# Performance work log

Measured on AMD Instinct MI355X. Metric: run time of the kernel, lower is better.

Reference implementation:

```python
import jax, jax.numpy as jnp
import numpy as np

BLOCK = 64          # block_size
R = 64              # number of OFT blocks (r)
N_ELEM = BLOCK * (BLOCK - 1) // 2  # 2016 upper-triangular elements per block
TOKENS = 8192       # batch*seq tokens
IN_FEATURES = R * BLOCK  # 4096
NUM_TERMS = 5       # num_cayley_neumann_terms

_ROWS, _COLS = jnp.triu_indices(BLOCK, k=1)


def _skew_symmetric(vec):
    # vec: [r, n_elements] -> [r, BLOCK, BLOCK] skew-symmetric
    m = jnp.zeros((vec.shape[0], BLOCK, BLOCK), dtype=vec.dtype)
    m = m.at[:, _ROWS, _COLS].set(vec)
    return m - jnp.swapaxes(m, -2, -1)


def _cayley_neumann(weight):
    # Neumann approximation of Cayley transform:
    # R = I + 2*Q + 2*Q^2 + ... + 2*Q^(NUM_TERMS-1)
    Q = _skew_symmetric(weight)                      # [r, B, B]
    eye = jnp.eye(BLOCK, dtype=weight.dtype)
    rot = eye[None, :, :] + 2.0 * Q
    Q_pow = Q
    for _ in range(2, NUM_TERMS):
        Q_pow = jnp.einsum('rij,rjk->rik', Q_pow, Q)
        rot = rot + 2.0 * Q_pow
    return rot                                        # [r, B, B]


def setup_inputs() -> dict:
    key = jax.random.key(0)
    k1, k2 = jax.random.split(key)
    x = jax.random.normal(k1, (TOKENS, IN_FEATURES), dtype=jnp.float32)
    # OFT weights start near zero (rotation ~ identity); small scale keeps
    # the Neumann series well-conditioned.
    weight = jax.random.normal(k2, (R, N_ELEM), dtype=jnp.float32) * 0.02
    return {"x": x, "weight": weight}


def reference(x, weight):
    rot = _cayley_neumann(weight)                      # [r, B, B]
    xr = x.reshape(x.shape[0], R, BLOCK)               # [n, r, B]
    out = jnp.einsum('nrk,rkc->nrc', xr, rot)          # block-diag rotation
    return out.reshape(x.shape)
```

## Files before the change

### kernel.cpp

```cpp
#include <hip/hip_runtime.h>


#define NELEM 2016

__device__ __forceinline__ int triu_off(int i) {
    return i * 63 - (i * (i - 1)) / 2;
}

__device__ __forceinline__ float skew_val(const float* __restrict__ wr, int i, int j) {
    if (i < j) return  wr[triu_off(i) + (j - i - 1)];
    if (i > j) return -wr[triu_off(j) + (i - j - 1)];
    return 0.f;
}

__global__ __launch_bounds__(256) void oft_rot_kernel(const float* __restrict__ w,
                                                      float* __restrict__ rot) {
    __shared__ float Q[64][64];
    __shared__ float Pl[2][16][65];

    const int r    = blockIdx.x;
    const int tile = blockIdx.y;
    const float* __restrict__ wr = w + r * NELEM;
    const int tid = threadIdx.x;
    const int il  = tid >> 4;
    const int j0  = (tid & 15) << 2;
    const int gi  = tile * 16 + il;

#pragma unroll
    for (int m = 0; m < 4; ++m) {
        const int i = il + 16 * m;
#pragma unroll
        for (int t = 0; t < 4; ++t)
            Q[i][j0 + t] = skew_val(wr, i, j0 + t);
    }
    __syncthreads();

    float racc[4];
#pragma unroll
    for (int t = 0; t < 4; ++t) {
        const float qv = Q[gi][j0 + t];
        Pl[0][il][j0 + t] = qv;
        racc[t] = (gi == j0 + t ? 1.f : 0.f) + 2.f * qv;
    }
    __syncthreads();

    int cur = 0;
#pragma unroll
    for (int p = 2; p < 5; ++p) {
        float a0 = 0.f, a1 = 0.f, a2 = 0.f, a3 = 0.f;
#pragma unroll 8
        for (int k = 0; k < 64; ++k) {
            const float  pv = Pl[cur][il][k];
            const float4 qv = *(const float4*)&Q[k][j0];
            a0 = fmaf(pv, qv.x, a0);
            a1 = fmaf(pv, qv.y, a1);
            a2 = fmaf(pv, qv.z, a2);
            a3 = fmaf(pv, qv.w, a3);
        }
        Pl[cur ^ 1][il][j0 + 0] = a0;
        Pl[cur ^ 1][il][j0 + 1] = a1;
        Pl[cur ^ 1][il][j0 + 2] = a2;
        Pl[cur ^ 1][il][j0 + 3] = a3;
        racc[0] += 2.f * a0;
        racc[1] += 2.f * a1;
        racc[2] += 2.f * a2;
        racc[3] += 2.f * a3;
        __syncthreads();
        cur ^= 1;
    }

    *(float4*)&rot[(size_t)r * 4096 + gi * 64 + j0] =
        make_float4(racc[0], racc[1], racc[2], racc[3]);
}

__global__ __launch_bounds__(256, 3) void oft_apply_kernel(const float* __restrict__ x,
                                                           const float* __restrict__ rot,
                                                           float* __restrict__ out) {
    __shared__ float rotS[64][64];
    __shared__ float xs[128][65];

    const int r   = blockIdx.x;
    const int tok0 = blockIdx.y * 128;
    const int tid = threadIdx.x;

    {
        const float4* __restrict__ src = (const float4*)(rot + (size_t)r * 4096);
        float4* dst = (float4*)&rotS[0][0];
#pragma unroll
        for (int p = 0; p < 4; ++p)
            dst[p * 256 + tid] = src[p * 256 + tid];
    }
#pragma unroll
    for (int p = 0; p < 8; ++p) {
        const int f   = p * 256 + tid;
        const int row = f >> 4;
        const int c   = (f & 15) << 2;
        const float4 v = *(const float4*)(x + (size_t)(tok0 + row) * 4096 + r * 64 + c);
        xs[row][c + 0] = v.x;
        xs[row][c + 1] = v.y;
        xs[row][c + 2] = v.z;
        xs[row][c + 3] = v.w;
    }
    __syncthreads();

    const int cq = tid & 15;
    const int tq = tid >> 4;
    const int c0 = cq << 2;
    const float* __restrict__ xbase = &xs[tq * 8][0];

    float acc[8][4];
#pragma unroll
    for (int m = 0; m < 8; ++m)
#pragma unroll
        for (int t = 0; t < 4; ++t) acc[m][t] = 0.f;

#pragma unroll 8
    for (int k = 0; k < 64; ++k) {
        const float4 rv = *(const float4*)&rotS[k][c0];
#pragma unroll
        for (int m = 0; m < 8; ++m) {
            const float xv = xbase[m * 65 + k];
            acc[m][0] = fmaf(xv, rv.x, acc[m][0]);
            acc[m][1] = fmaf(xv, rv.y, acc[m][1]);
            acc[m][2] = fmaf(xv, rv.z, acc[m][2]);
            acc[m][3] = fmaf(xv, rv.w, acc[m][3]);
        }
    }

#pragma unroll
    for (int m = 0; m < 8; ++m) {
        const int n = tok0 + tq * 8 + m;
        *(float4*)(out + (size_t)n * 4096 + r * 64 + c0) =
            make_float4(acc[m][0], acc[m][1], acc[m][2], acc[m][3]);
    }
}

extern "C" void kernel_launch(void* const* d_in, const int* in_sizes, int n_in,
                              void* d_out, int out_size, void* d_ws, size_t ws_size,
                              hipStream_t stream) {
    const float* x = (const float*)d_in[0];
    const float* w = (const float*)d_in[1];
    float* out = (float*)d_out;
    float* rot = (float*)d_ws;

    oft_rot_kernel<<<dim3(64, 4), 256, 0, stream>>>(w, rot);
    oft_apply_kernel<<<dim3(64, 64), 256, 0, stream>>>(x, rot, out);
}
```

Before: 250.0 us.

## Use split-bf16 MFMA for block-diagonal rotation apply with prepacked fragments

The rotation kernel now writes each rotation matrix as high and low bf16 halves, prepacked in MFMA B-fragment layout. The apply kernel drops the shared-memory fp32 FMA loop. Each wave loads x straight into registers, splits it into bf16 hi/lo, and runs three bf16 MFMA products per k-slab (hi*hi + hi*lo + lo*hi) to keep close to fp32 accuracy on matrix cores. This trades extra MFMA work and scattered scalar output stores for removing the LDS staging and scalar FMA throughput limits.

Result: no change. 253.6 us (+1.4%).

```diff
diff --git a/kernel.cpp b/kernel.cpp
--- a/kernel.cpp
+++ b/kernel.cpp
@@ -2,6 +2,9 @@
 
 
 #define NELEM 2016
+
+typedef __attribute__((ext_vector_type(8))) short bfrag8;
+typedef __attribute__((ext_vector_type(4))) float f32x4;
 
 __device__ __forceinline__ int triu_off(int i) {
     return i * 63 - (i * (i - 1)) / 2;
@@ -13,8 +16,17 @@
     return 0.f;
 }
 
+__device__ __forceinline__ void bsplit(float v, short& h, short& l) {
+    const unsigned u = __float_as_uint(v);
+    h = (short)(u >> 16);
+    const float resid = v - __uint_as_float(u & 0xffff0000u);
+    const unsigned ur = __float_as_uint(resid);
+    l = (short)((ur + 0x7fffu + ((ur >> 16) & 1u)) >> 16);
+}
+
 __global__ __launch_bounds__(256) void oft_rot_kernel(const float* __restrict__ w,
-                                                      float* __restrict__ rot) {
+                                                      unsigned short* __restrict__ bh,
+                                                      unsigned short* __restrict__ bl) {
     __shared__ float Q[64][64];
     __shared__ float Pl[2][16][65];
 
@@ -69,69 +81,83 @@
         cur ^= 1;
     }
 
-    *(float4*)&rot[(size_t)r * 4096 + gi * 64 + j0] =
-        make_float4(racc[0], racc[1], racc[2], racc[3]);
+    const int s    = gi >> 5;
+    const int jj   = gi & 7;
+    const int lhi  = ((gi >> 3) & 3) << 4;
+#pragma unroll
+    for (int t = 0; t < 4; ++t) {
+        const int j    = j0 + t;
+        const int ct   = j >> 4;
+        const int lane = lhi + (j & 15);
+        const int off  = (((r * 4 + ct) * 2 + s) * 64 + lane) * 8 + jj;
+        short h, l;
+        bsplit(racc[t], h, l);
+        bh[off] = (unsigned short)h;
+        bl[off] = (unsigned short)l;
+    }
 }
 
-__global__ __launch_bounds__(256, 3) void oft_apply_kernel(const float* __restrict__ x,
-                                                           const float* __restrict__ rot,
-                                                           float* __restrict__ out) {
-    __shared__ float rotS[64][64];
-    __shared__ float xs[128][65];
+__global__ __launch_bounds__(256) void oft_apply_kernel(const float* __restrict__ x,
+                                                        const unsigned short* __restrict__ bh,
+                                                        const unsigned short* __restrict__ bl,
+                                                        float* __restrict__ out) {
+    const int tid  = threadIdx.x;
+    const int w    = tid >> 6;
+    const int l    = tid & 63;
+    const int lrow = l & 15;
+    const int lk   = l >> 4;
+    const int r     = blockIdx.x;
+    const int chunk = blockIdx.y;
 
-    const int r   = blockIdx.x;
-    const int tok0 = blockIdx.y * 128;
-    const int tid = threadIdx.x;
-
-    {
-        const float4* __restrict__ src = (const float4*)(rot + (size_t)r * 4096);
-        float4* dst = (float4*)&rotS[0][0];
+    bfrag8 Bh[4][2], Bl[4][2];
 #pragma unroll
-        for (int p = 0; p < 4; ++p)
-            dst[p * 256 + tid] = src[p * 256 + tid];
-    }
+    for (int ct = 0; ct < 4; ++ct)
 #pragma unroll
-    for (int p = 0; p < 8; ++p) {
-        const int f   = p * 256 + tid;
-        const int row = f >> 4;
-        const int c   = (f & 15) << 2;
-        const float4 v = *(const float4*)(x + (size_t)(tok0 + row) * 4096 + r * 64 + c);
-        xs[row][c + 0] = v.x;
-        xs[row][c + 1] = v.y;
-        xs[row][c + 2] = v.z;
-        xs[row][c + 3] = v.w;
-    }
-    __syncthreads();
-
-    const int cq = tid & 15;
-    const int tq = tid >> 4;
-    const int c0 = cq << 2;
-    const float* __restrict__ xbase = &xs[tq * 8][0];
-
-    float acc[8][4];
-#pragma unroll
-    for (int m = 0; m < 8; ++m)
-#pragma unroll
-        for (int t = 0; t < 4; ++t) acc[m][t] = 0.f;
-
-#pragma unroll 8
-    for (int k = 0; k < 64; ++k) {
-        const float4 rv = *(const float4*)&rotS[k][c0];
-#pragma unroll
-        for (int m = 0; m < 8; ++m) {
-            const float xv = xbase[m * 65 + k];
-            acc[m][0] = fmaf(xv, rv.x, acc[m][0]);
-            acc[m][1] = fmaf(xv, rv.y, acc[m][1]);
-            acc[m][2] = fmaf(xv, rv.z, acc[m][2]);
-            acc[m][3] = fmaf(xv, rv.w, acc[m][3]);
+        for (int s = 0; s < 2; ++s) {
+            const int off = (((r * 4 + ct) * 2 + s) * 64 + l) * 8;
+            Bh[ct][s] = *(const bfrag8*)(bh + off);
+            Bl[ct][s] = *(const bfrag8*)(bl + off);
         }
-    }
 
 #pragma unroll
-    for (int m = 0; m < 8; ++m) {
-        const int n = tok0 + tq * 8 + m;
-        *(float4*)(out + (size_t)n * 4096 + r * 64 + c0) =
-            make_float4(acc[m][0], acc[m][1], acc[m][2], acc[m][3]);
+    for (int tt = 0; tt < 4; ++tt) {
+        const int tokbase = (chunk * 4 + tt) * 64 + w * 16;
+        const float* __restrict__ xp =
+            x + (size_t)(tokbase + lrow) * 4096 + r * 64 + lk * 8;
+
+        const f32x4 a0 = *(const f32x4*)(xp);
+        const f32x4 a1 = *(const f32x4*)(xp + 4);
+        const f32x4 a2 = *(const f32x4*)(xp + 32);
+        const f32x4 a3 = *(const f32x4*)(xp + 36);
+
+        bfrag8 Ah0, Al0, Ah1, Al1;
+#pragma unroll
+        for (int j = 0; j < 4; ++j) {
+            short h, lo;
+            bsplit(a0[j], h, lo); Ah0[j]     = h; Al0[j]     = lo;
+            bsplit(a1[j], h, lo); Ah0[4 + j] = h; Al0[4 + j] = lo;
+            bsplit(a2[j], h, lo); Ah1[j]     = h; Al1[j]     = lo;
+            bsplit(a3[j], h, lo); Ah1[4 + j] = h; Al1[4 + j] = lo;
+        }
+
+        f32x4 acc[4];
+#pragma unroll
+        for (int ct = 0; ct < 4; ++ct) {
+            acc[ct] = (f32x4)(0.f);
+            acc[ct] = __builtin_amdgcn_mfma_f32_16x16x32_bf16(Al0, Bh[ct][0], acc[ct], 0, 0, 0);
+            acc[ct] = __builtin_amdgcn_mfma_f32_16x16x32_bf16(Ah0, Bl[ct][0], acc[ct], 0, 0, 0);
+            acc[ct] = __builtin_amdgcn_mfma_f32_16x16x32_bf16(Ah0, Bh[ct][0], acc[ct], 0, 0, 0);
+            acc[ct] = __builtin_amdgcn_mfma_f32_16x16x32_bf16(Al1, Bh[ct][1], acc[ct], 0, 0, 0);
+            acc[ct] = __builtin_amdgcn_mfma_f32_16x16x32_bf16(Ah1, Bl[ct][1], acc[ct], 0, 0, 0);
+            acc[ct] = __builtin_amdgcn_mfma_f32_16x16x32_bf16(Ah1, Bh[ct][1], acc[ct], 0, 0, 0);
+        }
+
+        const size_t obase = (size_t)(tokbase + lk * 4) * 4096 + r * 64 + lrow;
+#pragma unroll
+        for (int ct = 0; ct < 4; ++ct)
+#pragma unroll
+            for (int q = 0; q < 4; ++q)
+                out[obase + (size_t)q * 4096 + ct * 16] = acc[ct][q];
     }
 }
 
@@ -141,8 +167,10 @@
     const float* x = (const float*)d_in[0];
     const float* w = (const float*)d_in[1];
     float* out = (float*)d_out;
-    float* rot = (float*)d_ws;
 
-    oft_rot_kernel<<<dim3(64, 4), 256, 0, stream>>>(w, rot);
-    oft_apply_kernel<<<dim3(64, 64), 256, 0, stream>>>(x, rot, out);
+    unsigned short* bh = (unsigned short*)d_ws;
+    unsigned short* bl = bh + 64 * 4 * 2 * 64 * 8;
+
+    oft_rot_kernel<<<dim3(64, 4), 256, 0, stream>>>(w, bh, bl);
+    oft_apply_kernel<<<dim3(64, 32), 256, 0, stream>>>(x, bh, bl, out);
 }
```
